# Performance work log

Measured on AMD Instinct MI355X. Metric: run time of the kernel, lower is better.

## Reference

```python
import jax, jax.numpy as jnp
import numpy as np

H = 128  # hidden_dim
COORD_CLAMP = 100.0


def _glorot(key, shape):
    fan_in, fan_out = shape[0], shape[1]
    lim = float(np.sqrt(6.0 / (fan_in + fan_out)))
    return jax.random.uniform(key, shape, jnp.float32, -lim, lim)


def setup_inputs() -> dict:
    key = jax.random.key(0)
    ks = jax.random.split(key, 20)
    B, N = 2, 512
    inp = {
        "h": jax.random.normal(ks[0], (B, N, H), jnp.float32),
        "pos": jax.random.normal(ks[1], (B, N, 3), jnp.float32),
        "vel": jax.random.normal(ks[2], (B, N, 3), jnp.float32),
        # edge_mlp: Linear(2H+2 -> H), SiLU, Linear(H -> H), SiLU
        "We1": _glorot(ks[3], (2 * H + 2, H)), "be1": jnp.zeros((H,), jnp.float32),
        "We2": _glorot(ks[4], (H, H)), "be2": jnp.zeros((H,), jnp.float32),
        # attention_mlp: Linear(H -> 1), Sigmoid
        "Wa": _glorot(ks[5], (H, 1)), "ba": jnp.zeros((1,), jnp.float32),
        # pos_mlp: Linear(H -> H), SiLU, Linear(H -> 1, no bias)
        "Wp1": _glorot(ks[6], (H, H)), "bp1": jnp.zeros((H,), jnp.float32),
        "Wp2": _glorot(ks[7], (H, 1)),
        # vel_mlp: Linear(H -> H), SiLU, Linear(H -> 1, no bias)
        "Wv1": _glorot(ks[8], (H, H)), "bv1": jnp.zeros((H,), jnp.float32),
        "Wv2": _glorot(ks[9], (H, 1)),
        # node_mlp: Linear(2H -> H), SiLU, Linear(H -> H)
        "Wn1": _glorot(ks[10], (2 * H, H)), "bn1": jnp.zeros((H,), jnp.float32),
        "Wn2": _glorot(ks[11], (H, H)), "bn2": jnp.zeros((H,), jnp.float32),
    }
    return inp


def reference(h, pos, vel, We1, be1, We2, be2, Wa, ba,
              Wp1, bp1, Wp2, Wv1, bv1, Wv2, Wn1, bn1, Wn2, bn2):
    B, N, _ = pos.shape
    # pairwise diffs: [B, N, N, 3]
    pos_diff = pos[:, :, None, :] - pos[:, None, :, :]
    vel_diff = vel[:, :, None, :] - vel[:, None, :, :]
    pos_dist_sq = jnp.sum(pos_diff ** 2, axis=-1, keepdims=True)  # [B,N,N,1]
    vel_dist_sq = jnp.sum(vel_diff ** 2, axis=-1, keepdims=True)
    h_i = jnp.broadcast_to(h[:, :, None, :], (B, N, N, H))
    h_j = jnp.broadcast_to(h[:, None, :, :], (B, N, N, H))
    edge_input = jnp.concatenate([h_i, h_j, pos_dist_sq, vel_dist_sq], axis=-1)  # [B,N,N,2H+2]
    # edge MLP
    m = jax.nn.silu(jnp.einsum('bijc,ch->bijh', edge_input, We1) + be1)
    m_ij = jax.nn.silu(jnp.einsum('bijh,hk->bijk', m, We2) + be2)
    # attention gate
    att = jax.nn.sigmoid(jnp.einsum('bijh,ho->bijo', m_ij, Wa) + ba)  # [B,N,N,1]
    m_ij = m_ij * att
    # tanh-weighted coordinate/velocity updates
    pos_w = jnp.tanh(jnp.einsum('bijh,ho->bijo', jax.nn.silu(jnp.einsum('bijh,hk->bijk', m_ij, Wp1) + bp1), Wp2))
    vel_w = jnp.tanh(jnp.einsum('bijh,ho->bijo', jax.nn.silu(jnp.einsum('bijh,hk->bijk', m_ij, Wv1) + bv1), Wv2))
    denom = jnp.float32(max(N - 1, 1))
    pos_update = jnp.sum(pos_diff * pos_w, axis=2) / denom  # [B,N,3]
    vel_update = jnp.sum(vel_diff * vel_w, axis=2) / denom
    pos_out = jnp.clip(pos + pos_update, -COORD_CLAMP, COORD_CLAMP)
    vel_out = jnp.clip(vel + vel_update, -COORD_CLAMP, COORD_CLAMP)
    # node update
    m_agg = jnp.sum(m_ij, axis=2)  # [B,N,H]
    node_input = jnp.concatenate([h, m_agg], axis=-1)  # [B,N,2H]
    h_out = jax.nn.silu(jnp.einsum('bnc,ch->bnh', node_input, Wn1) + bn1)
    h_out = jnp.einsum('bnh,hk->bnk', h_out, Wn2) + bn2
    h_out = h + h_out  # residual
    return (h_out, pos_out, vel_out)
```

## Files before the change

kernel.cpp:

```cpp
#include <hip/hip_runtime.h>
#include <hip/hip_bf16.h>
#include <hip/hip_cooperative_groups.h>

namespace cg = cooperative_groups;

#define Hd 128
#define Nn 512
#define TJ 32
#define LSTRIDE 136

typedef __bf16 bf16x8 __attribute__((ext_vector_type(8)));
typedef __bf16 bf16x4 __attribute__((ext_vector_type(4)));
typedef float  floatx4 __attribute__((ext_vector_type(4)));

__device__ __forceinline__ float frcp(float x){ return __builtin_amdgcn_rcpf(x); }
__device__ __forceinline__ float fsilu(float x){ return x * frcp(1.f + __expf(-x)); }
__device__ __forceinline__ float fsigm(float x){ return frcp(1.f + __expf(-x)); }
__device__ __forceinline__ float ftanh(float x){ return 1.f - 2.f * frcp(__expf(2.f*x) + 1.f); }
__device__ __forceinline__ float rfl(float x){
  return __int_as_float(__builtin_amdgcn_readfirstlane(__float_as_int(x)));
}

__device__ __forceinline__ void gemm_kloopT(const __bf16* __restrict__ buf,
                                            const bf16x8* __restrict__ Ws,
                                            int w, int lane, int q, int l15,
                                            floatx4 acc[2][2]){
  const floatx4 zero = {0.f, 0.f, 0.f, 0.f};
  #pragma unroll
  for (int m = 0; m < 2; ++m){ acc[m][0] = zero; acc[m][1] = zero; }
  #pragma unroll
  for (int s = 0; s < 4; ++s){
    bf16x8 bf[2];
    #pragma unroll
    for (int n = 0; n < 2; ++n)
      bf[n] = *(const bf16x8*)&buf[(16*n + l15)*LSTRIDE + s*32 + q*8];
    const bf16x8 a0 = Ws[((2*w + 0)*4 + s)*64 + lane];
    const bf16x8 a1 = Ws[((2*w + 1)*4 + s)*64 + lane];
    #pragma unroll
    for (int n = 0; n < 2; ++n){
      acc[0][n] = __builtin_amdgcn_mfma_f32_16x16x32_bf16(a0, bf[n], acc[0][n], 0, 0, 0);
      acc[1][n] = __builtin_amdgcn_mfma_f32_16x16x32_bf16(a1, bf[n], acc[1][n], 0, 0, 0);
    }
  }
}

__device__ __forceinline__ void wdotT(floatx4 acc[2][2], float att0, float att1,
                                      const float* __restrict__ biasL,
                                      const float* __restrict__ w2L,
                                      int w, int lane, int q, int l15,
                                      float (*part)[TJ]){
  const int fb0 = 32*w + 4*q, fb1 = fb0 + 16;
  const floatx4 bb0 = *(const floatx4*)&biasL[fb0];
  const floatx4 bb1 = *(const floatx4*)&biasL[fb1];
  const floatx4 w0  = *(const floatx4*)&w2L[fb0];
  const floatx4 w1  = *(const floatx4*)&w2L[fb1];
  float p0 = 0.f, p1 = 0.f;
  #pragma unroll
  for (int r = 0; r < 4; ++r){
    p0 += fsilu(fmaf(att0, acc[0][0][r], bb0[r])) * w0[r];
    p0 += fsilu(fmaf(att0, acc[1][0][r], bb1[r])) * w1[r];
    p1 += fsilu(fmaf(att1, acc[0][1][r], bb0[r])) * w0[r];
    p1 += fsilu(fmaf(att1, acc[1][1][r], bb1[r])) * w1[r];
  }
  p0 += __shfl_xor(p0, 16, 64); p0 += __shfl_xor(p0, 32, 64);
  p1 += __shfl_xor(p1, 16, 64); p1 += __shfl_xor(p1, 32, 64);
  if (lane < 16){
    part[w][l15]      = p0;
    part[w][16 + l15] = p1;
  }
}

__global__ __launch_bounds__(256) void egnn_coop(
    const float* __restrict__ h,
    const float* __restrict__ pos, const float* __restrict__ vel,
    const float* __restrict__ We1, const float* __restrict__ be1,
    const float* __restrict__ be2,
    const float* __restrict__ Wa,  const float* __restrict__ ba,
    const float* __restrict__ bp1, const float* __restrict__ Wp2,
    const float* __restrict__ bv1, const float* __restrict__ Wv2,
    const float* __restrict__ Wn1, const float* __restrict__ bn1,
    const float* __restrict__ Wn2, const float* __restrict__ bn2,
    const float* __restrict__ We2, const float* __restrict__ Wp1,
    const float* __restrict__ Wv1,
    float* __restrict__ Bm, __bf16* __restrict__ Wsw,
    float* __restrict__ out){

  const int t    = threadIdx.x;
  const int w    = t >> 6;
  const int lane = t & 63;
  const int q    = lane >> 4;
  const int l15  = lane & 15;
  const int node = blockIdx.x;
  const int b    = node >> 9;

  __shared__ float AiL[Hd], wpL[Hd], wvL[Hd];
  __shared__ float be2L[Hd], bp1L[Hd], bv1L[Hd], WaL[Hd], Wp2L[Hd], Wv2L[Hd];
  __shared__ __align__(16) __bf16 bufm [TJ*LSTRIDE];
  __shared__ __align__(16) __bf16 bufij[TJ*LSTRIDE];
  __shared__ float partAtt[4][TJ], partP[4][TJ], partV[4][TJ];
  __shared__ float attL[TJ];

  {
    const int k = t & 127, ch = t >> 7;
    if (t < Hd) AiL[t] = h[(size_t)node*Hd + t];
    __syncthreads();
    float a = 0.f, bm = 0.f;
    const int cb = ch*64;
    #pragma unroll 4
    for (int cc = 0; cc < 64; ++cc){
      const int c = cb + cc;
      const float hv = AiL[c];
      a  += hv * We1[c*Hd + k];
      bm += hv * We1[(c + Hd)*Hd + k];
    }
    float* pa = (float*)bufm;
    float* pb = pa + 256;
    pa[ch*128 + k] = a;
    pb[ch*128 + k] = bm;
    __syncthreads();
    if (t < Hd){
      const float av = pa[t] + pa[128 + t] + be1[t];
      Bm[(size_t)node*Hd + t] = pb[t] + pb[128 + t];
      AiL[t] = av;
    }
    if (node < 24){
      const int which = node >> 3, m = node & 7;
      const float* src = (which == 0) ? We2 : (which == 1 ? Wp1 : Wv1);
      __bf16* d = Wsw + which * (Hd*Hd);
      #pragma unroll
      for (int it = 0; it < 8; ++it){
        const int sidx = m*2048 + it*256 + t;
        const int kk = sidx >> 7, cc2 = sidx & 127;
        const int s = kk >> 5, j = kk & 7;
        const int ln = ((kk >> 3) & 3)*16 + (cc2 & 15);
        const int n = cc2 >> 4;
        d[n*2048 + s*512 + ln*8 + j] = (__bf16)src[sidx];
      }
    }
  }
  cg::this_grid().sync();

  if (t < Hd){
    wpL[t]  = We1[256*Hd + t];
    wvL[t]  = We1[257*Hd + t];
    be2L[t] = be2[t]; bp1L[t] = bp1[t]; bv1L[t] = bv1[t];
    WaL[t]  = Wa[t];  Wp2L[t] = Wp2[t]; Wv2L[t] = Wv2[t];
  }
  const float baV = ba[0];
  const float* pi = &pos[(size_t)node*3];
  const float* vi = &vel[(size_t)node*3];
  const float px = rfl(pi[0]), py = rfl(pi[1]), pz = rfl(pi[2]);
  const float ux = rfl(vi[0]), uy = rfl(vi[1]), uz = rfl(vi[2]);
  __syncthreads();

  const bf16x8* We2s = (const bf16x8*)(Wsw);
  const bf16x8* Wp1s = (const bf16x8*)(Wsw + Hd*Hd);
  const bf16x8* Wv1s = (const bf16x8*)(Wsw + 2*Hd*Hd);

  float accR[8];
  #pragma unroll
  for (int e = 0; e < 8; ++e) accR[e] = 0.f;

  for (int jt = 0; jt < Nn/TJ; ++jt){
    const int j0 = jt * TJ;

    {
      const int g  = t & 15;
      const int j2 = t >> 4;
      const floatx4 a0 = *(const floatx4*)&AiL[g*8];
      const floatx4 a1 = *(const floatx4*)&AiL[g*8 + 4];
      const floatx4 p0 = *(const floatx4*)&wpL[g*8];
      const floatx4 p1 = *(const floatx4*)&wpL[g*8 + 4];
      const floatx4 v0 = *(const floatx4*)&wvL[g*8];
      const floatx4 v1 = *(const floatx4*)&wvL[g*8 + 4];
      #pragma unroll
      for (int rr = 0; rr < 2; ++rr){
        const int j = j2 + rr*16;
        const int jg = j0 + j;
        const float* pj = &pos[(size_t)(b*Nn + jg)*3];
        const float* vj = &vel[(size_t)(b*Nn + jg)*3];
        const float dx = px - pj[0], dy = py - pj[1], dz = pz - pj[2];
        const float dp = dx*dx + dy*dy + dz*dz;
        const float ex = ux - vj[0], ey = uy - vj[1], ez = uz - vj[2];
        const float dv = ex*ex + ey*ey + ez*ez;
        const floatx4* Bp4 = (const floatx4*)&Bm[((size_t)(b*Nn + jg))*Hd + g*8];
        const floatx4 b0 = Bp4[0], b1 = Bp4[1];
        union { bf16x8 v; __hip_bfloat162 h2[4]; } o;
        float x[8];
        #pragma unroll
        for (int e = 0; e < 4; ++e){
          x[e]   = fsilu(a0[e] + b0[e] + dp*p0[e] + dv*v0[e]);
          x[4+e] = fsilu(a1[e] + b1[e] + dp*p1[e] + dv*v1[e]);
        }
        o.h2[0] = __float22bfloat162_rn(make_float2(x[0], x[1]));
        o.h2[1] = __float22bfloat162_rn(make_float2(x[2], x[3]));
        o.h2[2] = __float22bfloat162_rn(make_float2(x[4], x[5]));
        o.h2[3] = __float22bfloat162_rn(make_float2(x[6], x[7]));
        *(bf16x8*)&bufm[j*LSTRIDE + g*8] = o.v;
      }
    }
    __syncthreads();

    {
      floatx4 acc[2][2];
      gemm_kloopT(bufm, We2s, w, lane, q, l15, acc);
      const int fb0 = 32*w + 4*q, fb1 = fb0 + 16;
      const floatx4 be0 = *(const floatx4*)&be2L[fb0];
      const floatx4 be1v = *(const floatx4*)&be2L[fb1];
      const floatx4 wa0 = *(const floatx4*)&WaL[fb0];
      const floatx4 wa1 = *(const floatx4*)&WaL[fb1];
      float aw[2];
      #pragma unroll
      for (int n = 0; n < 2; ++n){
        const int j = 16*n + l15;
        float s0[4], s1[4];
        #pragma unroll
        for (int r = 0; r < 4; ++r){
          s0[r] = fsilu(acc[0][n][r] + be0[r]);
          s1[r] = fsilu(acc[1][n][r] + be1v[r]);
        }
        aw[n] = s0[0]*wa0[0] + s0[1]*wa0[1] + s0[2]*wa0[2] + s0[3]*wa0[3]
              + s1[0]*wa1[0] + s1[1]*wa1[1] + s1[2]*wa1[2] + s1[3]*wa1[3];
        union { bf16x4 v; __hip_bfloat162 h2[2]; } p0k, p1k;
        p0k.h2[0] = __float22bfloat162_rn(make_float2(s0[0], s0[1]));
        p0k.h2[1] = __float22bfloat162_rn(make_float2(s0[2], s0[3]));
        p1k.h2[0] = __float22bfloat162_rn(make_float2(s1[0], s1[1]));
        p1k.h2[1] = __float22bfloat162_rn(make_float2(s1[2], s1[3]));
        *(bf16x4*)&bufij[j*LSTRIDE + fb0] = p0k.v;
        *(bf16x4*)&bufij[j*LSTRIDE + fb1] = p1k.v;
      }
      aw[0] += __shfl_xor(aw[0], 16, 64); aw[0] += __shfl_xor(aw[0], 32, 64);
      aw[1] += __shfl_xor(aw[1], 16, 64); aw[1] += __shfl_xor(aw[1], 32, 64);
      if (lane < 16){
        partAtt[w][l15]      = aw[0];
        partAtt[w][16 + l15] = aw[1];
      }
    }
    __syncthreads();

    {
      const float att0 = fsigm(partAtt[0][l15] + partAtt[1][l15] +
                               partAtt[2][l15] + partAtt[3][l15] + baV);
      const float att1 = fsigm(partAtt[0][16+l15] + partAtt[1][16+l15] +
                               partAtt[2][16+l15] + partAtt[3][16+l15] + baV);
      if (w == 0 && lane < 16){ attL[l15] = att0; attL[16 + l15] = att1; }
      floatx4 acc[2][2];
      gemm_kloopT(bufij, Wp1s, w, lane, q, l15, acc);
      wdotT(acc, att0, att1, bp1L, Wp2L, w, lane, q, l15, partP);
      gemm_kloopT(bufij, Wv1s, w, lane, q, l15, acc);
      wdotT(acc, att0, att1, bv1L, Wv2L, w, lane, q, l15, partV);
    }
    __syncthreads();

    if (w == 0){
      if (lane < TJ){
        const int jg = j0 + lane;
        const float* pj = &pos[(size_t)(b*Nn + jg)*3];
        const float s4 = partP[0][lane] + partP[1][lane] + partP[2][lane] + partP[3][lane];
        const float pw = ftanh(s4);
        accR[0] += (px - pj[0]) * pw;
        accR[1] += (py - pj[1]) * pw;
        accR[2] += (pz - pj[2]) * pw;
      }
    } else if (w == 1){
      if (lane < TJ){
        const int jg = j0 + lane;
        const float* vj = &vel[(size_t)(b*Nn + jg)*3];
        const float s4 = partV[0][lane] + partV[1][lane] + partV[2][lane] + partV[3][lane];
        const float vw = ftanh(s4);
        accR[0] += (ux - vj[0]) * vw;
        accR[1] += (uy - vj[1]) * vw;
        accR[2] += (uz - vj[2]) * vw;
      }
    } else {
      const int sg   = (w - 2)*8 + (lane & 7);
      const int jsub = lane >> 3;
      #pragma unroll
      for (int jj = 0; jj < 4; ++jj){
        const int j = jj*8 + jsub;
        const float aj = attL[j];
        const bf16x8 v = *(const bf16x8*)&bufij[j*LSTRIDE + sg*8];
        #pragma unroll
        for (int e = 0; e < 8; ++e) accR[e] += aj * (float)v[e];
      }
    }
  }

  float* sF = (float*)bufm;
  if (t < Hd) sF[t] = h[(size_t)node*Hd + t];

  if (w == 0 || w == 1){
    float v0 = accR[0], v1 = accR[1], v2 = accR[2];
    #pragma unroll
    for (int off = 1; off < 64; off <<= 1){
      v0 += __shfl_xor(v0, off, 64);
      v1 += __shfl_xor(v1, off, 64);
      v2 += __shfl_xor(v2, off, 64);
    }
    if (lane == 0){
      const float inv = 1.f / 511.f;
      if (w == 0){
        float o0 = pi[0] + v0*inv, o1 = pi[1] + v1*inv, o2 = pi[2] + v2*inv;
        out[2*Nn*Hd + node*3 + 0] = fminf(fmaxf(o0, -100.f), 100.f);
        out[2*Nn*Hd + node*3 + 1] = fminf(fmaxf(o1, -100.f), 100.f);
        out[2*Nn*Hd + node*3 + 2] = fminf(fmaxf(o2, -100.f), 100.f);
      } else {
        float o0 = vi[0] + v0*inv, o1 = vi[1] + v1*inv, o2 = vi[2] + v2*inv;
        out[2*Nn*Hd + 2*Nn*3 + node*3 + 0] = fminf(fmaxf(o0, -100.f), 100.f);
        out[2*Nn*Hd + 2*Nn*3 + node*3 + 1] = fminf(fmaxf(o1, -100.f), 100.f);
        out[2*Nn*Hd + 2*Nn*3 + node*3 + 2] = fminf(fmaxf(o2, -100.f), 100.f);
      }
    }
  } else {
    const int sg = (w - 2)*8 + (lane & 7);
    #pragma unroll
    for (int off = 8; off < 64; off <<= 1){
      #pragma unroll
      for (int e = 0; e < 8; ++e) accR[e] += __shfl_xor(accR[e], off, 64);
    }
    if ((lane >> 3) == 0){
      *(float4*)&sF[128 + sg*8 + 0] = make_float4(accR[0], accR[1], accR[2], accR[3]);
      *(float4*)&sF[128 + sg*8 + 4] = make_float4(accR[4], accR[5], accR[6], accR[7]);
    }
  }
  __syncthreads();

  {
    const int k = t & 127, ch = t >> 7;
    const int cb = ch*Hd;
    float a0=0.f,a1=0.f,a2=0.f,a3=0.f;
    #pragma unroll 8
    for (int cc = 0; cc < Hd; cc += 4){
      a0 += sF[cb+cc+0] * Wn1[(cb+cc+0)*Hd + k];
      a1 += sF[cb+cc+1] * Wn1[(cb+cc+1)*Hd + k];
      a2 += sF[cb+cc+2] * Wn1[(cb+cc+2)*Hd + k];
      a3 += sF[cb+cc+3] * Wn1[(cb+cc+3)*Hd + k];
    }
    sF[256 + ch*128 + k] = (a0+a1)+(a2+a3);
  }
  __syncthreads();
  if (t < Hd) sF[512 + t] = fsilu(sF[256 + t] + sF[384 + t] + bn1[t]);
  __syncthreads();
  {
    const int k = t & 127, ch = t >> 7;
    const int cb = ch*64;
    float a0=0.f,a1=0.f,a2=0.f,a3=0.f;
    #pragma unroll 8
    for (int cc = 0; cc < 64; cc += 4){
      a0 += sF[512+cb+cc+0] * Wn2[(cb+cc+0)*Hd + k];
      a1 += sF[512+cb+cc+1] * Wn2[(cb+cc+1)*Hd + k];
      a2 += sF[512+cb+cc+2] * Wn2[(cb+cc+2)*Hd + k];
      a3 += sF[512+cb+cc+3] * Wn2[(cb+cc+3)*Hd + k];
    }
    sF[256 + ch*128 + k] = (a0+a1)+(a2+a3);
  }
  __syncthreads();
  if (t < Hd)
    out[(size_t)node*Hd + t] = sF[t] + sF[256 + t] + sF[384 + t] + bn2[t];
}

__global__ __launch_bounds__(256) void prep(const float* __restrict__ h,
                                            const float* __restrict__ We1,
                                            const float* __restrict__ be1,
                                            const float* __restrict__ We2,
                                            const float* __restrict__ Wp1,
                                            const float* __restrict__ Wv1,
                                            float* __restrict__ A,
                                            float* __restrict__ Bm,
                                            __bf16* __restrict__ dst,
                                            float* __restrict__ zbase){
  if (blockIdx.x < 256){
    const int r0 = blockIdx.x * 4;
    const int k = threadIdx.x & 127, ch = threadIdx.x >> 7;
    __shared__ float hL[4][Hd];
    __shared__ float pa[2][4][Hd], pb[2][4][Hd];
    for (int idx = threadIdx.x; idx < 4*Hd; idx += 256)
      hL[idx >> 7][idx & 127] = h[r0*Hd + idx];
    __syncthreads();
    float a[4] = {0.f,0.f,0.f,0.f}, bb[4] = {0.f,0.f,0.f,0.f};
    const int cbase = ch*64;
    #pragma unroll 4
    for (int cc = 0; cc < 64; ++cc){
      const int c = cbase + cc;
      const float wa = We1[c*Hd + k];
      const float wb = We1[(c + Hd)*Hd + k];
      #pragma unroll
      for (int rr = 0; rr < 4; ++rr){
        a[rr]  += hL[rr][c] * wa;
        bb[rr] += hL[rr][c] * wb;
      }
    }
    #pragma unroll
    for (int rr = 0; rr < 4; ++rr){ pa[ch][rr][k] = a[rr]; pb[ch][rr][k] = bb[rr]; }
    __syncthreads();
    if (threadIdx.x < Hd){
      const float be = be1[k];
      #pragma unroll
      for (int rr = 0; rr < 4; ++rr){
        A[(r0+rr)*Hd + k]  = pa[0][rr][k] + pa[1][rr][k] + be;
        Bm[(r0+rr)*Hd + k] = pb[0][rr][k] + pb[1][rr][k];
      }
    }
  } else if (blockIdx.x < 280){
    const int blk = blockIdx.x - 256;
    const int which = blk >> 3, m = blk & 7;
    const float* src = (which == 0) ? We2 : (which == 1 ? Wp1 : Wv1);
    __bf16* d = dst + which * (Hd*Hd);
    #pragma unroll
    for (int it = 0; it < 8; ++it){
      const int sidx = m*2048 + it*256 + threadIdx.x;
      const int kk = sidx >> 7, cc = sidx & 127;
      const int s = kk >> 5, j = kk & 7;
      const int lane = ((kk >> 3) & 3)*16 + (cc & 15);
      const int n = cc >> 4;
      d[n*2048 + s*512 + lane*8 + j] = (__bf16)src[sidx];
    }
  } else {
    const int t0 = (blockIdx.x - 280)*256 + threadIdx.x;
    for (int idx = t0; idx < 137216; idx += 2048) zbase[idx] = 0.f;
  }
}

__global__ __launch_bounds__(256) void egnn_main(
    const float* __restrict__ pos, const float* __restrict__ vel,
    const float* __restrict__ We1, const float* __restrict__ be2,
    const float* __restrict__ Wa,  const float* __restrict__ ba,
    const float* __restrict__ bp1, const float* __restrict__ Wp2,
    const float* __restrict__ bv1, const float* __restrict__ Wv2,
    const float* __restrict__ A,   const float* __restrict__ Bm,
    const __bf16* __restrict__ Wsw,
    float* __restrict__ magg, float* __restrict__ posu, float* __restrict__ velu){

  const int t    = threadIdx.x;
  const int w    = t >> 6;
  const int lane = t & 63;
  const int q    = lane >> 4;
  const int l15  = lane & 15;
  const int node = blockIdx.x >> 1;
  const int half = blockIdx.x & 1;
  const int b    = node >> 9;

  __shared__ float AiL[Hd], wpL[Hd], wvL[Hd];
  __shared__ float be2L[Hd], bp1L[Hd], bv1L[Hd], WaL[Hd], Wp2L[Hd], Wv2L[Hd];
  __shared__ __align__(16) __bf16 bufm [TJ*LSTRIDE];
  __shared__ __align__(16) __bf16 bufij[TJ*LSTRIDE];
  __shared__ float partAtt[4][TJ], partP[4][TJ], partV[4][TJ];
  __shared__ float attL[TJ];

  if (t < Hd){
    AiL[t]  = A[node*Hd + t];
    wpL[t]  = We1[256*Hd + t];
    wvL[t]  = We1[257*Hd + t];
    be2L[t] = be2[t]; bp1L[t] = bp1[t]; bv1L[t] = bv1[t];
    WaL[t]  = Wa[t];  Wp2L[t] = Wp2[t]; Wv2L[t] = Wv2[t];
  }
  const float baV = ba[0];
  const float* pi = &pos[(size_t)node*3];
  const float* vi = &vel[(size_t)node*3];
  const float px = rfl(pi[0]), py = rfl(pi[1]), pz = rfl(pi[2]);
  const float ux = rfl(vi[0]), uy = rfl(vi[1]), uz = rfl(vi[2]);
  __syncthreads();

  const bf16x8* We2s = (const bf16x8*)(Wsw);
  const bf16x8* Wp1s = (const bf16x8*)(Wsw + Hd*Hd);
  const bf16x8* Wv1s = (const bf16x8*)(Wsw + 2*Hd*Hd);

  float accR[8];
  #pragma unroll
  for (int e = 0; e < 8; ++e) accR[e] = 0.f;

  for (int jt = 0; jt < (Nn/2)/TJ; ++jt){
    const int j0 = half*(Nn/2) + jt * TJ;
    {
      const int g  = t & 15;
      const int j2 = t >> 4;
      const floatx4 a0 = *(const floatx4*)&AiL[g*8];
      const floatx4 a1 = *(const floatx4*)&AiL[g*8 + 4];
      const floatx4 p0 = *(const floatx4*)&wpL[g*8];
      const floatx4 p1 = *(const floatx4*)&wpL[g*8 + 4];
      const floatx4 v0 = *(const floatx4*)&wvL[g*8];
      const floatx4 v1 = *(const floatx4*)&wvL[g*8 + 4];
      #pragma unroll
      for (int rr = 0; rr < 2; ++rr){
        const int j = j2 + rr*16;
        const int jg = j0 + j;
        const float* pj = &pos[(size_t)(b*Nn + jg)*3];
        const float* vj = &vel[(size_t)(b*Nn + jg)*3];
        const float dx = px - pj[0], dy = py - pj[1], dz = pz - pj[2];
        const float dp = dx*dx + dy*dy + dz*dz;
        const float ex = ux - vj[0], ey = uy - vj[1], ez = uz - vj[2];
        const float dv = ex*ex + ey*ey + ez*ez;
        const floatx4* Bp4 = (const floatx4*)&Bm[((size_t)(b*Nn + jg))*Hd + g*8];
        const floatx4 b0 = Bp4[0], b1 = Bp4[1];
        union { bf16x8 v; __hip_bfloat162 h2[4]; } o;
        float x[8];
        #pragma unroll
        for (int e = 0; e < 4; ++e){
          x[e]   = fsilu(a0[e] + b0[e] + dp*p0[e] + dv*v0[e]);
          x[4+e] = fsilu(a1[e] + b1[e] + dp*p1[e] + dv*v1[e]);
        }
        o.h2[0] = __float22bfloat162_rn(make_float2(x[0], x[1]));
        o.h2[1] = __float22bfloat162_rn(make_float2(x[2], x[3]));
        o.h2[2] = __float22bfloat162_rn(make_float2(x[4], x[5]));
        o.h2[3] = __float22bfloat162_rn(make_float2(x[6], x[7]));
        *(bf16x8*)&bufm[j*LSTRIDE + g*8] = o.v;
      }
    }
    __syncthreads();
    {
      floatx4 acc[2][2];
      gemm_kloopT(bufm, We2s, w, lane, q, l15, acc);
      const int fb0 = 32*w + 4*q, fb1 = fb0 + 16;
      const floatx4 be0 = *(const floatx4*)&be2L[fb0];
      const floatx4 be1v = *(const floatx4*)&be2L[fb1];
      const floatx4 wa0 = *(const floatx4*)&WaL[fb0];
      const floatx4 wa1 = *(const floatx4*)&WaL[fb1];
      float aw[2];
      #pragma unroll
      for (int n = 0; n < 2; ++n){
        const int j = 16*n + l15;
        float s0[4], s1[4];
        #pragma unroll
        for (int r = 0; r < 4; ++r){
          s0[r] = fsilu(acc[0][n][r] + be0[r]);
          s1[r] = fsilu(acc[1][n][r] + be1v[r]);
        }
        aw[n] = s0[0]*wa0[0] + s0[1]*wa0[1] + s0[2]*wa0[2] + s0[3]*wa0[3]
              + s1[0]*wa1[0] + s1[1]*wa1[1] + s1[2]*wa1[2] + s1[3]*wa1[3];
        union { bf16x4 v; __hip_bfloat162 h2[2]; } p0k, p1k;
        p0k.h2[0] = __float22bfloat162_rn(make_float2(s0[0], s0[1]));
        p0k.h2[1] = __float22bfloat162_rn(make_float2(s0[2], s0[3]));
        p1k.h2[0] = __float22bfloat162_rn(make_float2(s1[0], s1[1]));
        p1k.h2[1] = __float22bfloat162_rn(make_float2(s1[2], s1[3]));
        *(bf16x4*)&bufij[j*LSTRIDE + fb0] = p0k.v;
        *(bf16x4*)&bufij[j*LSTRIDE + fb1] = p1k.v;
      }
      aw[0] += __shfl_xor(aw[0], 16, 64); aw[0] += __shfl_xor(aw[0], 32, 64);
      aw[1] += __shfl_xor(aw[1], 16, 64); aw[1] += __shfl_xor(aw[1], 32, 64);
      if (lane < 16){
        partAtt[w][l15]      = aw[0];
        partAtt[w][16 + l15] = aw[1];
      }
    }
    __syncthreads();
    {
      const float att0 = fsigm(partAtt[0][l15] + partAtt[1][l15] +
                               partAtt[2][l15] + partAtt[3][l15] + baV);
      const float att1 = fsigm(partAtt[0][16+l15] + partAtt[1][16+l15] +
                               partAtt[2][16+l15] + partAtt[3][16+l15] + baV);
      if (w == 0 && lane < 16){ attL[l15] = att0; attL[16 + l15] = att1; }
      floatx4 acc[2][2];
      gemm_kloopT(bufij, Wp1s, w, lane, q, l15, acc);
      wdotT(acc, att0, att1, bp1L, Wp2L, w, lane, q, l15, partP);
      gemm_kloopT(bufij, Wv1s, w, lane, q, l15, acc);
      wdotT(acc, att0, att1, bv1L, Wv2L, w, lane, q, l15, partV);
    }
    __syncthreads();
    if (w == 0){
      if (lane < TJ){
        const int jg = j0 + lane;
        const float* pj = &pos[(size_t)(b*Nn + jg)*3];
        const float s4 = partP[0][lane] + partP[1][lane] + partP[2][lane] + partP[3][lane];
        const float pw = ftanh(s4);
        accR[0] += (px - pj[0]) * pw;
        accR[1] += (py - pj[1]) * pw;
        accR[2] += (pz - pj[2]) * pw;
      }
    } else if (w == 1){
      if (lane < TJ){
        const int jg = j0 + lane;
        const float* vj = &vel[(size_t)(b*Nn + jg)*3];
        const float s4 = partV[0][lane] + partV[1][lane] + partV[2][lane] + partV[3][lane];
        const float vw = ftanh(s4);
        accR[0] += (ux - vj[0]) * vw;
        accR[1] += (uy - vj[1]) * vw;
        accR[2] += (uz - vj[2]) * vw;
      }
    } else {
      const int sg   = (w - 2)*8 + (lane & 7);
      const int jsub = lane >> 3;
      #pragma unroll
      for (int jj = 0; jj < 4; ++jj){
        const int j = jj*8 + jsub;
        const float aj = attL[j];
        const bf16x8 v = *(const bf16x8*)&bufij[j*LSTRIDE + sg*8];
        #pragma unroll
        for (int e = 0; e < 8; ++e) accR[e] += aj * (float)v[e];
      }
    }
  }

  if (w == 0 || w == 1){
    float v0 = accR[0], v1 = accR[1], v2 = accR[2];
    #pragma unroll
    for (int off = 1; off < 64; off <<= 1){
      v0 += __shfl_xor(v0, off, 64);
      v1 += __shfl_xor(v1, off, 64);
      v2 += __shfl_xor(v2, off, 64);
    }
    if (lane == 0){
      float* dst = (w == 0) ? &posu[node*3] : &velu[node*3];
      atomicAdd(&dst[0], v0);
      atomicAdd(&dst[1], v1);
      atomicAdd(&dst[2], v2);
    }
  } else {
    const int sg = (w - 2)*8 + (lane & 7);
    #pragma unroll
    for (int off = 8; off < 64; off <<= 1){
      #pragma unroll
      for (int e = 0; e < 8; ++e) accR[e] += __shfl_xor(accR[e], off, 64);
    }
    if ((lane >> 3) == 0){
      #pragma unroll
      for (int e = 0; e < 8; ++e)
        atomicAdd(&magg[node*Hd + sg*8 + e], accR[e]);
    }
  }
}

__global__ __launch_bounds__(256) void egnn_final(
    const float* __restrict__ h, const float* __restrict__ pos, const float* __restrict__ vel,
    const float* __restrict__ Wn1, const float* __restrict__ bn1,
    const float* __restrict__ Wn2, const float* __restrict__ bn2,
    const float* __restrict__ magg, const float* __restrict__ posu,
    const float* __restrict__ velu, float* __restrict__ out){
  const int row = blockIdx.x;
  const int t = threadIdx.x;
  const int k = t & 127, ch = t >> 7;
  __shared__ float ni[2*Hd];
  __shared__ float p1[2][Hd], t1[Hd];
  ni[t] = (t < Hd) ? h[row*Hd + t] : magg[row*Hd + (t - Hd)];
  __syncthreads();
  {
    float a0=0.f,a1=0.f,a2=0.f,a3=0.f;
    const int cb = ch*Hd;
    #pragma unroll 8
    for (int cc = 0; cc < Hd; cc += 4){
      a0 += ni[cb+cc+0] * Wn1[(cb+cc+0)*Hd + k];
      a1 += ni[cb+cc+1] * Wn1[(cb+cc+1)*Hd + k];
      a2 += ni[cb+cc+2] * Wn1[(cb+cc+2)*Hd + k];
      a3 += ni[cb+cc+3] * Wn1[(cb+cc+3)*Hd + k];
    }
    p1[ch][k] = (a0+a1)+(a2+a3);
  }
  __syncthreads();
  if (t < Hd) t1[t] = fsilu(p1[0][t] + p1[1][t] + bn1[t]);
  __syncthreads();
  {
    float a0=0.f,a1=0.f,a2=0.f,a3=0.f;
    const int cb = ch*64;
    #pragma unroll 8
    for (int cc = 0; cc < 64; cc += 4){
      a0 += t1[cb+cc+0] * Wn2[(cb+cc+0)*Hd + k];
      a1 += t1[cb+cc+1] * Wn2[(cb+cc+1)*Hd + k];
      a2 += t1[cb+cc+2] * Wn2[(cb+cc+2)*Hd + k];
      a3 += t1[cb+cc+3] * Wn2[(cb+cc+3)*Hd + k];
    }
    p1[ch][k] = (a0+a1)+(a2+a3);
  }
  __syncthreads();
  if (t < Hd){
    out[row*Hd + t] = ni[t] + p1[0][t] + p1[1][t] + bn2[t];
  } else if (t < Hd + 3){
    const int d = t - Hd;
    const float v = pos[row*3 + d] + posu[row*3 + d] * (1.f/511.f);
    out[2*Nn*Hd + row*3 + d] = fminf(fmaxf(v, -100.f), 100.f);
  } else if (t < Hd + 6){
    const int d = t - Hd - 3;
    const float v = vel[row*3 + d] + velu[row*3 + d] * (1.f/511.f);
    out[2*Nn*Hd + 2*Nn*3 + row*3 + d] = fminf(fmaxf(v, -100.f), 100.f);
  }
}

extern "C" void kernel_launch(void* const* d_in, const int* in_sizes, int n_in,
                              void* d_out, int out_size, void* d_ws, size_t ws_size,
                              hipStream_t stream){
  const float* h   = (const float*)d_in[0];
  const float* pos = (const float*)d_in[1];
  const float* vel = (const float*)d_in[2];
  const float* We1 = (const float*)d_in[3];
  const float* be1 = (const float*)d_in[4];
  const float* We2 = (const float*)d_in[5];
  const float* be2 = (const float*)d_in[6];
  const float* Wa  = (const float*)d_in[7];
  const float* ba  = (const float*)d_in[8];
  const float* Wp1 = (const float*)d_in[9];
  const float* bp1 = (const float*)d_in[10];
  const float* Wp2 = (const float*)d_in[11];
  const float* Wv1 = (const float*)d_in[12];
  const float* bv1 = (const float*)d_in[13];
  const float* Wv2 = (const float*)d_in[14];
  const float* Wn1 = (const float*)d_in[15];
  const float* bn1 = (const float*)d_in[16];
  const float* Wn2 = (const float*)d_in[17];
  const float* bn2 = (const float*)d_in[18];

  float* ws = (float*)d_ws;
  float*  A    = ws;
  float*  Bmm  = ws + 131072;
  float*  magg = ws + 262144;
  float*  posu = ws + 393216;
  float*  velu = ws + 396288;
  __bf16* Wsw  = (__bf16*)(ws + 399360);
  float*  outp = (float*)d_out;

  int maxB = 0;
  hipError_t qe = hipOccupancyMaxActiveBlocksPerMultiprocessor(
      &maxB, (const void*)egnn_coop, 256, 0);
  const bool coop = (qe == hipSuccess && maxB >= 4);

  if (coop){
    void* args[] = {
      (void*)&h, (void*)&pos, (void*)&vel, (void*)&We1, (void*)&be1,
      (void*)&be2, (void*)&Wa, (void*)&ba, (void*)&bp1, (void*)&Wp2,
      (void*)&bv1, (void*)&Wv2, (void*)&Wn1, (void*)&bn1, (void*)&Wn2,
      (void*)&bn2, (void*)&We2, (void*)&Wp1, (void*)&Wv1,
      (void*)&Bmm, (void*)&Wsw, (void*)&outp
    };
    hipLaunchCooperativeKernel((const void*)egnn_coop, dim3(1024), dim3(256),
                               args, 0, stream);
  } else {
    prep      <<<dim3(288),  dim3(256), 0, stream>>>(h, We1, be1, We2, Wp1, Wv1,
                                                     A, Bmm, Wsw, magg);
    egnn_main <<<dim3(2048), dim3(256), 0, stream>>>(pos, vel, We1, be2, Wa, ba, bp1, Wp2,
                                                     bv1, Wv2, A, Bmm, Wsw, magg, posu, velu);
    egnn_final<<<dim3(1024), dim3(256), 0, stream>>>(h, pos, vel, Wn1, bn1, Wn2, bn2,
                                                     magg, posu, velu, outp);
  }
}
```

Measured before the change: 232.1 us.

## Replace cooperative grid sync with separate prep kernel plus fused edge kernel

New measurement: 234.6 us. No clear change (+1.1%).

```diff
diff --git a/kernel.cpp b/kernel.cpp
--- a/kernel.cpp
+++ b/kernel.cpp
@@ -1,8 +1,5 @@
 #include <hip/hip_runtime.h>
 #include <hip/hip_bf16.h>
-#include <hip/hip_cooperative_groups.h>
-
-namespace cg = cooperative_groups;
 
 #define Hd 128
 #define Nn 512
@@ -19,6 +16,68 @@
 __device__ __forceinline__ float ftanh(float x){ return 1.f - 2.f * frcp(__expf(2.f*x) + 1.f); }
 __device__ __forceinline__ float rfl(float x){
   return __int_as_float(__builtin_amdgcn_readfirstlane(__float_as_int(x)));
+}
+
+__global__ __launch_bounds__(256) void prep(const float* __restrict__ h,
+                                            const float* __restrict__ We1,
+                                            const float* __restrict__ be1,
+                                            const float* __restrict__ We2,
+                                            const float* __restrict__ Wp1,
+                                            const float* __restrict__ Wv1,
+                                            float* __restrict__ A,
+                                            float* __restrict__ Bm,
+                                            __bf16* __restrict__ dst,
+                                            float* __restrict__ zbase){
+  if (blockIdx.x < 256){
+    const int r0 = blockIdx.x * 4;
+    const int k = threadIdx.x & 127, ch = threadIdx.x >> 7;
+    __shared__ float hL[4][Hd];
+    __shared__ float pa[2][4][Hd], pb[2][4][Hd];
+    for (int idx = threadIdx.x; idx < 4*Hd; idx += 256)
+      hL[idx >> 7][idx & 127] = h[r0*Hd + idx];
+    __syncthreads();
+    float a[4] = {0.f,0.f,0.f,0.f}, bb[4] = {0.f,0.f,0.f,0.f};
+    const int cbase = ch*64;
+    #pragma unroll 4
+    for (int cc = 0; cc < 64; ++cc){
+      const int c = cbase + cc;
+      const float wa = We1[c*Hd + k];
+      const float wb = We1[(c + Hd)*Hd + k];
+      #pragma unroll
+      for (int rr = 0; rr < 4; ++rr){
+        a[rr]  += hL[rr][c] * wa;
+        bb[rr] += hL[rr][c] * wb;
+      }
+    }
+    #pragma unroll
+    for (int rr = 0; rr < 4; ++rr){ pa[ch][rr][k] = a[rr]; pb[ch][rr][k] = bb[rr]; }
+    __syncthreads();
+    if (threadIdx.x < Hd){
+      const float be = be1[k];
+      #pragma unroll
+      for (int rr = 0; rr < 4; ++rr){
+        A[(r0+rr)*Hd + k]  = pa[0][rr][k] + pa[1][rr][k] + be;
+        Bm[(r0+rr)*Hd + k] = pb[0][rr][k] + pb[1][rr][k];
+      }
+    }
+  } else if (blockIdx.x < 280){
+    const int blk = blockIdx.x - 256;
+    const int which = blk >> 3, m = blk & 7;
+    const float* src = (which == 0) ? We2 : (which == 1 ? Wp1 : Wv1);
+    __bf16* d = dst + which * (Hd*Hd);
+    #pragma unroll
+    for (int it = 0; it < 8; ++it){
+      const int sidx = m*2048 + it*256 + threadIdx.x;
+      const int kk = sidx >> 7, cc = sidx & 127;
+      const int s = kk >> 5, j = kk & 7;
+      const int lane = ((kk >> 3) & 3)*16 + (cc & 15);
+      const int n = cc >> 4;
+      d[n*2048 + s*512 + lane*8 + j] = (__bf16)src[sidx];
+    }
+  } else {
+    const int t0 = (blockIdx.x - 280)*256 + threadIdx.x;
+    for (int idx = t0; idx < 137216; idx += 2048) zbase[idx] = 0.f;
+  }
 }
 
 __device__ __forceinline__ void gemm_kloopT(const __bf16* __restrict__ buf,
@@ -70,19 +129,17 @@
   }
 }
 
-__global__ __launch_bounds__(256) void egnn_coop(
+__global__ __launch_bounds__(256) void egnn_fused(
     const float* __restrict__ h,
     const float* __restrict__ pos, const float* __restrict__ vel,
-    const float* __restrict__ We1, const float* __restrict__ be1,
-    const float* __restrict__ be2,
+    const float* __restrict__ We1, const float* __restrict__ be2,
     const float* __restrict__ Wa,  const float* __restrict__ ba,
     const float* __restrict__ bp1, const float* __restrict__ Wp2,
     const float* __restrict__ bv1, const float* __restrict__ Wv2,
     const float* __restrict__ Wn1, const float* __restrict__ bn1,
     const float* __restrict__ Wn2, const float* __restrict__ bn2,
-    const float* __restrict__ We2, const float* __restrict__ Wp1,
-    const float* __restrict__ Wv1,
-    float* __restrict__ Bm, __bf16* __restrict__ Wsw,
+    const float* __restrict__ A,   const float* __restrict__ Bm,
+    const __bf16* __restrict__ Wsw,
     float* __restrict__ out){
 
   const int t    = threadIdx.x;
@@ -99,48 +156,11 @@
   __shared__ __align__(16) __bf16 bufij[TJ*LSTRIDE];
   __shared__ float partAtt[4][TJ], partP[4][TJ], partV[4][TJ];
   __shared__ float attL[TJ];
-
-  {
-    const int k = t & 127, ch = t >> 7;
-    if (t < Hd) AiL[t] = h[(size_t)node*Hd + t];
-    __syncthreads();
-    float a = 0.f, bm = 0.f;
-    const int cb = ch*64;
-    #pragma unroll 4
-    for (int cc = 0; cc < 64; ++cc){
-      const int c = cb + cc;
-      const float hv = AiL[c];
-      a  += hv * We1[c*Hd + k];
-      bm += hv * We1[(c + Hd)*Hd + k];
-    }
-    float* pa = (float*)bufm;
-    float* pb = pa + 256;
-    pa[ch*128 + k] = a;
-    pb[ch*128 + k] = bm;
-    __syncthreads();
-    if (t < Hd){
-      const float av = pa[t] + pa[128 + t] + be1[t];
-      Bm[(size_t)node*Hd + t] = pb[t] + pb[128 + t];
-      AiL[t] = av;
-    }
-    if (node < 24){
-      const int which = node >> 3, m = node & 7;
-      const float* src = (which == 0) ? We2 : (which == 1 ? Wp1 : Wv1);
-      __bf16* d = Wsw + which * (Hd*Hd);
-      #pragma unroll
-      for (int it = 0; it < 8; ++it){
-        const int sidx = m*2048 + it*256 + t;
-        const int kk = sidx >> 7, cc2 = sidx & 127;
-        const int s = kk >> 5, j = kk & 7;
-        const int ln = ((kk >> 3) & 3)*16 + (cc2 & 15);
-        const int n = cc2 >> 4;
-        d[n*2048 + s*512 + ln*8 + j] = (__bf16)src[sidx];
-      }
-    }
-  }
-  cg::this_grid().sync();
+  __shared__ float sMag[Hd];
+  __shared__ float sRed[8];
 
   if (t < Hd){
+    AiL[t]  = A[(size_t)node*Hd + t];
     wpL[t]  = We1[256*Hd + t];
     wvL[t]  = We1[257*Hd + t];
     be2L[t] = be2[t]; bp1L[t] = bp1[t]; bv1L[t] = bv1[t];
@@ -163,7 +183,6 @@
 
   for (int jt = 0; jt < Nn/TJ; ++jt){
     const int j0 = jt * TJ;
-
     {
       const int g  = t & 15;
       const int j2 = t >> 4;
@@ -200,7 +219,6 @@
       }
     }
     __syncthreads();
-
     {
       floatx4 acc[2][2];
       gemm_kloopT(bufm, We2s, w, lane, q, l15, acc);
@@ -237,7 +255,6 @@
       }
     }
     __syncthreads();
-
     {
       const float att0 = fsigm(partAtt[0][l15] + partAtt[1][l15] +
                                partAtt[2][l15] + partAtt[3][l15] + baV);
@@ -251,7 +268,6 @@
       wdotT(acc, att0, att1, bv1L, Wv2L, w, lane, q, l15, partV);
     }
     __syncthreads();
-
     if (w == 0){
       if (lane < TJ){
         const int jg = j0 + lane;
@@ -286,9 +302,6 @@
     }
   }
 
-  float* sF = (float*)bufm;
-  if (t < Hd) sF[t] = h[(size_t)node*Hd + t];
-
   if (w == 0 || w == 1){
     float v0 = accR[0], v1 = accR[1], v2 = accR[2];
     #pragma unroll
@@ -298,18 +311,8 @@
       v2 += __shfl_xor(v2, off, 64);
     }
     if (lane == 0){
-      const float inv = 1.f / 511.f;
-      if (w == 0){
-        float o0 = pi[0] + v0*inv, o1 = pi[1] + v1*inv, o2 = pi[2] + v2*inv;
-        out[2*Nn*Hd + node*3 + 0] = fminf(fmaxf(o0, -100.f), 100.f);
-        out[2*Nn*Hd + node*3 + 1] = fminf(fmaxf(o1, -100.f), 100.f);
-        out[2*Nn*Hd + node*3 + 2] = fminf(fmaxf(o2, -100.f), 100.f);
-      } else {
-        float o0 = vi[0] + v0*inv, o1 = vi[1] + v1*inv, o2 = vi[2] + v2*inv;
-        out[2*Nn*Hd + 2*Nn*3 + node*3 + 0] = fminf(fmaxf(o0, -100.f), 100.f);
-        out[2*Nn*Hd + 2*Nn*3 + node*3 + 1] = fminf(fmaxf(o1, -100.f), 100.f);
-        out[2*Nn*Hd + 2*Nn*3 + node*3 + 2] = fminf(fmaxf(o2, -100.f), 100.f);
-      }
+      float* dst = (w == 0) ? &sRed[0] : &sRed[3];
+      dst[0] = v0; dst[1] = v1; dst[2] = v2;
     }
   } else {
     const int sg = (w - 2)*8 + (lane & 7);
@@ -319,12 +322,26 @@
       for (int e = 0; e < 8; ++e) accR[e] += __shfl_xor(accR[e], off, 64);
     }
     if ((lane >> 3) == 0){
-      *(float4*)&sF[128 + sg*8 + 0] = make_float4(accR[0], accR[1], accR[2], accR[3]);
-      *(float4*)&sF[128 + sg*8 + 4] = make_float4(accR[4], accR[5], accR[6], accR[7]);
-    }
-  }
-  __syncthreads();
-
+      *(float4*)&sMag[sg*8 + 0] = make_float4(accR[0], accR[1], accR[2], accR[3]);
+      *(float4*)&sMag[sg*8 + 4] = make_float4(accR[4], accR[5], accR[6], accR[7]);
+    }
+  }
+  __syncthreads();
+
+  float* sF = (float*)bufm;
+  if (t < Hd){
+    sF[t] = h[(size_t)node*Hd + t];
+    sF[128 + t] = sMag[t];
+  } else if (t < Hd + 3){
+    const int d = t - Hd;
+    const float o = pi[d] + sRed[d]*(1.f/511.f);
+    out[2*Nn*Hd + node*3 + d] = fminf(fmaxf(o, -100.f), 100.f);
+  } else if (t < Hd + 6){
+    const int d = t - Hd - 3;
+    const float o = vi[d] + sRed[3+d]*(1.f/511.f);
+    out[2*Nn*Hd + 2*Nn*3 + node*3 + d] = fminf(fmaxf(o, -100.f), 100.f);
+  }
+  __syncthreads();
   {
     const int k = t & 127, ch = t >> 7;
     const int cb = ch*Hd;
@@ -357,68 +374,6 @@
   __syncthreads();
   if (t < Hd)
     out[(size_t)node*Hd + t] = sF[t] + sF[256 + t] + sF[384 + t] + bn2[t];
-}
-
-__global__ __launch_bounds__(256) void prep(const float* __restrict__ h,
-                                            const float* __restrict__ We1,
-                                            const float* __restrict__ be1,
-                                            const float* __restrict__ We2,
-                                            const float* __restrict__ Wp1,
-                                            const float* __restrict__ Wv1,
-                                            float* __restrict__ A,
-                                            float* __restrict__ Bm,
-                                            __bf16* __restrict__ dst,
-                                            float* __restrict__ zbase){
-  if (blockIdx.x < 256){
-    const int r0 = blockIdx.x * 4;
-    const int k = threadIdx.x & 127, ch = threadIdx.x >> 7;
-    __shared__ float hL[4][Hd];
-    __shared__ float pa[2][4][Hd], pb[2][4][Hd];
-    for (int idx = threadIdx.x; idx < 4*Hd; idx += 256)
-      hL[idx >> 7][idx & 127] = h[r0*Hd + idx];
-    __syncthreads();
-    float a[4] = {0.f,0.f,0.f,0.f}, bb[4] = {0.f,0.f,0.f,0.f};
-    const int cbase = ch*64;
-    #pragma unroll 4
-    for (int cc = 0; cc < 64; ++cc){
-      const int c = cbase + cc;
-      const float wa = We1[c*Hd + k];
-      const float wb = We1[(c + Hd)*Hd + k];
-      #pragma unroll
-      for (int rr = 0; rr < 4; ++rr){
-        a[rr]  += hL[rr][c] * wa;
-        bb[rr] += hL[rr][c] * wb;
-      }
-    }
-    #pragma unroll
-    for (int rr = 0; rr < 4; ++rr){ pa[ch][rr][k] = a[rr]; pb[ch][rr][k] = bb[rr]; }
-    __syncthreads();
-    if (threadIdx.x < Hd){
-      const float be = be1[k];
-      #pragma unroll
-      for (int rr = 0; rr < 4; ++rr){
-        A[(r0+rr)*Hd + k]  = pa[0][rr][k] + pa[1][rr][k] + be;
-        Bm[(r0+rr)*Hd + k] = pb[0][rr][k] + pb[1][rr][k];
-      }
-    }
-  } else if (blockIdx.x < 280){
-    const int blk = blockIdx.x - 256;
-    const int which = blk >> 3, m = blk & 7;
-    const float* src = (which == 0) ? We2 : (which == 1 ? Wp1 : Wv1);
-    __bf16* d = dst + which * (Hd*Hd);
-    #pragma unroll
-    for (int it = 0; it < 8; ++it){
-      const int sidx = m*2048 + it*256 + threadIdx.x;
-      const int kk = sidx >> 7, cc = sidx & 127;
-      const int s = kk >> 5, j = kk & 7;
-      const int lane = ((kk >> 3) & 3)*16 + (cc & 15);
-      const int n = cc >> 4;
-      d[n*2048 + s*512 + lane*8 + j] = (__bf16)src[sidx];
-    }
-  } else {
-    const int t0 = (blockIdx.x - 280)*256 + threadIdx.x;
-    for (int idx = t0; idx < 137216; idx += 2048) zbase[idx] = 0.f;
-  }
 }
 
 __global__ __launch_bounds__(256) void egnn_main(
@@ -705,26 +660,19 @@
   __bf16* Wsw  = (__bf16*)(ws + 399360);
   float*  outp = (float*)d_out;
 
-  int maxB = 0;
-  hipError_t qe = hipOccupancyMaxActiveBlocksPerMultiprocessor(
-      &maxB, (const void*)egnn_coop, 256, 0);
-  const bool coop = (qe == hipSuccess && maxB >= 4);
-
-  if (coop){
-    void* args[] = {
-      (void*)&h, (void*)&pos, (void*)&vel, (void*)&We1, (void*)&be1,
-      (void*)&be2, (void*)&Wa, (void*)&ba, (void*)&bp1, (void*)&Wp2,
-      (void*)&bv1, (void*)&Wv2, (void*)&Wn1, (void*)&bn1, (void*)&Wn2,
-      (void*)&bn2, (void*)&We2, (void*)&Wp1, (void*)&Wv1,
-      (void*)&Bmm, (void*)&Wsw, (void*)&outp
-    };
-    hipLaunchCooperativeKernel((const void*)egnn_coop, dim3(1024), dim3(256),
-                               args, 0, stream);
+  hipFuncAttributes attr{};
+  hipError_t ae = hipFuncGetAttributes(&attr, (const void*)egnn_fused);
+  const bool useFused = (ae == hipSuccess && attr.numRegs > 0 && attr.numRegs <= 160);
+
+  prep<<<dim3(288), dim3(256), 0, stream>>>(h, We1, be1, We2, Wp1, Wv1,
+                                            A, Bmm, Wsw, magg);
+  if (useFused){
+    egnn_fused<<<dim3(1024), dim3(256), 0, stream>>>(h, pos, vel, We1, be2, Wa, ba,
+                                                     bp1, Wp2, bv1, Wv2, Wn1, bn1,
+                                                     Wn2, bn2, A, Bmm, Wsw, outp);
   } else {
-    prep      <<<dim3(288),  dim3(256), 0, stream>>>(h, We1, be1, We2, Wp1, Wv1,
-                                                     A, Bmm, Wsw, magg);
-    egnn_main <<<dim3(2048), dim3(256), 0, stream>>>(pos, vel, We1, be2, Wa, ba, bp1, Wp2,
-                                                     bv1, Wv2, A, Bmm, Wsw, magg, posu, velu);
+    egnn_main<<<dim3(2048), dim3(256), 0, stream>>>(pos, vel, We1, be2, Wa, ba, bp1, Wp2,
+                                                    bv1, Wv2, A, Bmm, Wsw, magg, posu, velu);
     egnn_final<<<dim3(1024), dim3(256), 0, stream>>>(h, pos, vel, Wn1, bn1, Wn2, bn2,
                                                      magg, posu, velu, outp);
   }
```
